# Kernel tuning notes

Hardware: AMD Instinct MI355X
Metric: run time of the kernel (lower is better)

Reference implementation:

```python
import jax, jax.numpy as jnp
import numpy as np


def hard_sigmoid(x):
    # Keras hard_sigmoid: clip(0.2*x + 0.5, 0, 1)
    return jnp.clip(0.2 * x + 0.5, 0.0, 1.0)


def lstm_layer(x, W, U, b):
    """Run a Keras-style LSTM cell over time.

    x: [B, T, D], W: [D, 4H], U: [H, 4H], b: [4H]. Gate order i,f,g,o.
    Returns full hidden sequence [B, T, H].
    """
    B = x.shape[0]
    H = U.shape[0]
    h0 = jnp.zeros((B, H), dtype=x.dtype)
    c0 = jnp.zeros((B, H), dtype=x.dtype)
    # Precompute input projections for all timesteps in one big GEMM.
    xz = jnp.einsum('btd,dk->btk', x, W) + b  # [B, T, 4H]
    xz_t = jnp.swapaxes(xz, 0, 1)             # [T, B, 4H]

    def step(carry, zx_t):
        h, c = carry
        z = zx_t + h @ U                       # [B, 4H]
        i, f, g, o = jnp.split(z, 4, axis=-1)
        i = hard_sigmoid(i)
        f = hard_sigmoid(f)
        g = jnp.tanh(g)
        o = hard_sigmoid(o)
        c = f * c + i * g
        h = o * jnp.tanh(c)
        return (h, c), h

    (_, _), hs = jax.lax.scan(step, (h0, c0), xz_t)  # hs: [T, B, H]
    return jnp.swapaxes(hs, 0, 1)  # [B, T, H]


def setup_inputs() -> dict:
    key = jax.random.key(0)
    ks = jax.random.split(key, 7)
    B, T, D, H = 32, 512, 1024, 1024
    s_in = 1.0 / np.sqrt(D)
    s_h = 1.0 / np.sqrt(H)
    return {
        'x': jax.random.normal(ks[0], (B, T, D), dtype=jnp.float32),
        'W0': jax.random.normal(ks[1], (D, 4 * H), dtype=jnp.float32) * s_in,
        'U0': jax.random.normal(ks[2], (H, 4 * H), dtype=jnp.float32) * s_h,
        'b0': jnp.zeros((4 * H,), dtype=jnp.float32),
        'W1': jax.random.normal(ks[3], (H, 4 * H), dtype=jnp.float32) * s_h,
        'U1': jax.random.normal(ks[4], (H, 4 * H), dtype=jnp.float32) * s_h,
        'b1': jnp.zeros((4 * H,), dtype=jnp.float32),
    }


def reference(x, W0, U0, b0, W1, U1, b1):
    # StackedRNNCells: output of cell 0 at time t feeds cell 1 at time t.
    # Equivalent to running layer 0 over the whole sequence, then layer 1.
    h1 = lstm_layer(x, W0, U0, b0)    # [B, T, H]
    h2 = lstm_layer(h1, W1, U1, b1)   # [B, T, H]
    # RNN(return_sequences=False): last timestep output of the top cell.
    return h2[:, -1, :]
```

## Files before the change

### kernel.cpp

```cpp
#include <hip/hip_runtime.h>
#include <math.h>

#define B_  32
#define T_  512
#define H_  1024
#define G4_ 4096
#define NT  512

typedef __attribute__((ext_vector_type(8))) _Float16 f16x8;
typedef __attribute__((ext_vector_type(4))) float   f32x4;

#define ROWP 1032
#define WROW 264

__device__ __forceinline__ float hardsig(float z) {
    return fminf(fmaxf(0.2f * z + 0.5f, 0.0f), 1.0f);
}
__device__ __forceinline__ float fast_tanh(float x) {
    float ax = fabsf(x);
    float e  = __expf(-2.0f * ax);
    float t  = (1.0f - e) / (1.0f + e);
    return copysignf(t, x);
}
__device__ __forceinline__ unsigned ldA(const unsigned* p) {
    return __hip_atomic_load(p, __ATOMIC_RELAXED, __HIP_MEMORY_SCOPE_AGENT);
}
__device__ __forceinline__ void stA32(unsigned* p, unsigned v) {
    __hip_atomic_store(p, v, __ATOMIC_RELAXED, __HIP_MEMORY_SCOPE_AGENT);
}

__device__ __forceinline__ void load_wfrags(const float* M, int colbase, int myrow,
                                            int koff, bool keep, f16x8* wf, _Float16* st) {
    for (int kc = 0; kc < 4; ++kc) {
        __syncthreads();
        #pragma unroll
        for (int it = 0; it < 4; ++it) {
            int id  = it * NT + (int)threadIdx.x;
            int kl  = id >> 3, gc8 = id & 7;
            int gcol = (gc8 >> 1) * 1024 + colbase + (gc8 & 1) * 8;
            const float* src = M + (size_t)(kc * 256 + kl) * G4_ + gcol;
            float4 v0 = *(const float4*)src;
            float4 v1 = *(const float4*)(src + 4);
            int rb = gc8 * 8;
            st[(rb+0)*WROW+kl]=(_Float16)v0.x; st[(rb+1)*WROW+kl]=(_Float16)v0.y;
            st[(rb+2)*WROW+kl]=(_Float16)v0.z; st[(rb+3)*WROW+kl]=(_Float16)v0.w;
            st[(rb+4)*WROW+kl]=(_Float16)v1.x; st[(rb+5)*WROW+kl]=(_Float16)v1.y;
            st[(rb+6)*WROW+kl]=(_Float16)v1.z; st[(rb+7)*WROW+kl]=(_Float16)v1.w;
        }
        __syncthreads();
        if (keep) {
            #pragma unroll
            for (int kj = 0; kj < 8; ++kj)
                wf[kc*8+kj] = *(const f16x8*)&st[myrow * WROW + kj * 32 + koff];
        }
    }
    __syncthreads();
}

__global__ __launch_bounds__(NT, 1)
void lstm3(const float* __restrict__ x,
           const float* __restrict__ W0, const float* __restrict__ U0, const float* __restrict__ b0,
           const float* __restrict__ W1, const float* __restrict__ U1, const float* __restrict__ b1,
           _Float16* __restrict__ h1,
           _Float16* __restrict__ h2,
           _Float16* __restrict__ xzr,
           const _Float16* __restrict__ zp,
           unsigned* __restrict__ ctr,
           float* __restrict__ out)
{
    __shared__ __align__(16) char smem[149504];
    _Float16* stA  = (_Float16*)smem;
    _Float16* stB  = (_Float16*)(smem + 66048);
    float*    red0 = (float*)(smem + 66048);
    float*    red1 = (float*)(smem + 132096);

    const int tid  = threadIdx.x;
    const int bid  = blockIdx.x;
    const int w    = tid >> 6, l = tid & 63;
    const int koff = (l >> 4) * 8;

    if (bid >= 128) {
        const int e = bid - 128;
        const int gbase = e * 32;
        _Float16* w0l = (_Float16*)smem;

        #pragma unroll 2
        for (int it = 0; it < 8; ++it) {
            int id = it * NT + tid;
            int k = id >> 2, gc8 = id & 3;
            const float* src = W0 + (size_t)k * G4_ + gbase + gc8 * 8;
            float4 v0 = *(const float4*)src;
            float4 v1 = *(const float4*)(src + 4);
            int rb = gc8 * 8;
            w0l[(rb+0)*ROWP+k]=(_Float16)v0.x; w0l[(rb+1)*ROWP+k]=(_Float16)v0.y;
            w0l[(rb+2)*ROWP+k]=(_Float16)v0.z; w0l[(rb+3)*ROWP+k]=(_Float16)v0.w;
            w0l[(rb+4)*ROWP+k]=(_Float16)v1.x; w0l[(rb+5)*ROWP+k]=(_Float16)v1.y;
            w0l[(rb+6)*ROWP+k]=(_Float16)v1.z; w0l[(rb+7)*ROWP+k]=(_Float16)v1.w;
        }
        __syncthreads();

        for (int c = 0; c < 64; ++c) {
            if (c >= 4 && tid == 0) {
                const unsigned need = (unsigned)(8 * c - 24);
                while (ldA(&ctr[64 + (e & 15) * 16]) < need) __builtin_amdgcn_s_sleep(1);
            }
            __syncthreads();

            f32x4 acc[2][2] = {{{0,0,0,0},{0,0,0,0}},{{0,0,0,0},{0,0,0,0}}};
            const float* xrow[2];
            #pragma unroll
            for (int p = 0; p < 2; ++p) {
                const int m  = (w * 2 + p) * 16 + (l & 15);
                const int tl = m >> 5, bb = m & 31;
                xrow[p] = x + ((size_t)bb * T_ + (8 * c + tl)) * 1024;
            }
            #pragma unroll 4
            for (int kiG = 0; kiG < 32; ++kiG) {
                const int kk = kiG * 32 + koff;
                f16x8 bf0 = *(const f16x8*)&w0l[( 0 + (l & 15)) * ROWP + kk];
                f16x8 bf1 = *(const f16x8*)&w0l[(16 + (l & 15)) * ROWP + kk];
                #pragma unroll
                for (int p = 0; p < 2; ++p) {
                    float4 v0 = *(const float4*)&xrow[p][kk];
                    float4 v1 = *(const float4*)&xrow[p][kk + 4];
                    f16x8 af;
                    af[0]=(_Float16)v0.x; af[1]=(_Float16)v0.y; af[2]=(_Float16)v0.z; af[3]=(_Float16)v0.w;
                    af[4]=(_Float16)v1.x; af[5]=(_Float16)v1.y; af[6]=(_Float16)v1.z; af[7]=(_Float16)v1.w;
                    acc[p][0] = __builtin_amdgcn_mfma_f32_16x16x32_f16(af, bf0, acc[p][0], 0, 0, 0);
                    acc[p][1] = __builtin_amdgcn_mfma_f32_16x16x32_f16(af, bf1, acc[p][1], 0, 0, 0);
                }
            }
            #pragma unroll
            for (int p = 0; p < 2; ++p)
                #pragma unroll
                for (int n = 0; n < 2; ++n)
                    #pragma unroll
                    for (int i = 0; i < 4; ++i) {
                        _Float16 hf = (_Float16)acc[p][n][i];
                        unsigned short us; __builtin_memcpy(&us, &hf, 2);
                        unsigned up = us;
                        unsigned op = (unsigned)__shfl_xor((int)up, 1);
                        if (!(l & 1)) {
                            const int m  = (w * 2 + p) * 16 + (l >> 4) * 4 + i;
                            const int tl = m >> 5, bb = m & 31;
                            size_t off = (((size_t)(c & 3) * 8 + tl) * B_ + bb) * G4_
                                       + gbase + n * 16 + (l & 15);
                            stA32((unsigned*)&xzr[off], up | (op << 16));
                        }
                    }
            asm volatile("s_waitcnt vmcnt(0)" ::: "memory");
            __syncthreads();
            if (tid == 0) {
                unsigned old = __hip_atomic_fetch_add(&ctr[32], 1u, __ATOMIC_RELAXED, __HIP_MEMORY_SCOPE_AGENT);
                if ((old & 127u) == 127u) {
                    #pragma unroll
                    for (int i = 0; i < 16; ++i) stA32(&ctr[576 + i * 16], (unsigned)(c + 1));
                }
            }
        }
        return;
    }

    const int dom  = (bid >= 64);
    const int dbid = bid & 63;
    const int jb   = dbid * 16;

    const int bb   = tid >> 4;
    const int jj   = tid & 15;
    const int jcol = jb + jj;

    float bias_[4];
    {
        const float* bl = dom ? b1 : b0;
        #pragma unroll
        for (int g = 0; g < 4; ++g) bias_[g] = bl[(size_t)g * H_ + jcol];
    }
    float creg = 0.f;

    f16x8 wf[32];
    if (dom == 0) {
        const int g = w & 3;
        load_wfrags(U0, jb, g * 16 + (l & 15), koff, true, wf, stA);
    } else {
        const int g = w & 3;
        load_wfrags(W1, jb, g * 16 + (l & 15), koff, (w < 4),  wf, stA);
        load_wfrags(U1, jb, g * 16 + (l & 15), koff, (w >= 4), wf, stA);
    }

    for (int t = 0; t < T_; ++t) {
        if (tid == 0) {
            if (dom == 0) {
                const unsigned xt = (unsigned)((t >> 3) + 1);
                while (ldA(&ctr[576 + (dbid & 15) * 16]) < xt) __builtin_amdgcn_s_sleep(1);
                if (t > 0)
                    while (ldA(&ctr[64 + (dbid & 15) * 16]) < (unsigned)t) __builtin_amdgcn_s_sleep(1);
            } else {
                while (ldA(&ctr[64 + (dbid & 15) * 16]) < (unsigned)(t + 1)) __builtin_amdgcn_s_sleep(1);
                if (t > 0)
                    while (ldA(&ctr[320 + (dbid & 15) * 16]) < (unsigned)t) __builtin_amdgcn_s_sleep(1);
            }
        }
        __syncthreads();

        {
            const int r = tid >> 4, ch = tid & 15;
            if (dom == 0) {
                const _Float16* s1 = (t ? h1 + ((size_t)(t-1) * B_ + r) * H_ : zp + (size_t)r * H_) + ch * 64;
                _Float16* d1 = stA + r * ROWP + ch * 64;
                #pragma unroll
                for (int u = 0; u < 8; ++u) *(uint4*)(d1 + u*8) = *(const uint4*)(s1 + u*8);
            } else {
                const _Float16* s1 = h1 + ((size_t)t * B_ + r) * H_ + ch * 64;
                const _Float16* s2 = (t ? h2 + ((size_t)(t-1) * B_ + r) * H_ : zp + (size_t)r * H_) + ch * 64;
                _Float16* d1 = stA + r * ROWP + ch * 64;
                _Float16* d2 = stB + r * ROWP + ch * 64;
                #pragma unroll
                for (int u = 0; u < 8; ++u) *(uint4*)(d1 + u*8) = *(const uint4*)(s1 + u*8);
                #pragma unroll
                for (int u = 0; u < 8; ++u) *(uint4*)(d2 + u*8) = *(const uint4*)(s2 + u*8);
            }
        }
        float xzv[4] = {0.f, 0.f, 0.f, 0.f};
        if (dom == 0) {
            const size_t base = (((size_t)((t >> 3) & 3) * 8 + (t & 7)) * B_ + bb) * G4_;
            #pragma unroll
            for (int g = 0; g < 4; ++g) {
                const unsigned* dp = (const unsigned*)&xzr[base + g * 1024 + (jcol & ~1)];
                unsigned dv = ldA(dp);
                unsigned short hb = (jcol & 1) ? (unsigned short)(dv >> 16) : (unsigned short)(dv & 0xffff);
                _Float16 hf; __builtin_memcpy(&hf, &hb, 2);
                xzv[g] = (float)hf;
            }
        }
        __syncthreads();

        if (dom == 0) {
            const int mt = w >> 2, g = w & 3;
            const _Float16* ar = stA + (mt * 16 + (l & 15)) * ROWP;
            f32x4 aE = {0,0,0,0}, aO = {0,0,0,0};
            #pragma unroll
            for (int kiG = 0; kiG < 32; kiG += 2) {
                f16x8 a0 = *(const f16x8*)&ar[kiG * 32 + koff];
                f16x8 a1 = *(const f16x8*)&ar[(kiG + 1) * 32 + koff];
                aE = __builtin_amdgcn_mfma_f32_16x16x32_f16(a0, wf[kiG],   aE, 0, 0, 0);
                aO = __builtin_amdgcn_mfma_f32_16x16x32_f16(a1, wf[kiG+1], aO, 0, 0, 0);
            }
            f32x4 acc = aE + aO;
            #pragma unroll
            for (int i = 0; i < 4; ++i)
                red0[((mt * 4 + g) * 16 + (l >> 4) * 4 + i) * 17 + (l & 15)] = acc[i];
        } else {
            const int rl = w >> 2, g = w & 3;
            const _Float16* ab = rl ? stB : stA;
            f32x4 ac0 = {0,0,0,0}, ac1 = {0,0,0,0};
            #pragma unroll
            for (int kiG = 0; kiG < 32; ++kiG) {
                const int kk = kiG * 32 + koff;
                f16x8 bfr = wf[kiG];
                f16x8 a0 = *(const f16x8*)&ab[( 0 + (l & 15)) * ROWP + kk];
                f16x8 a1 = *(const f16x8*)&ab[(16 + (l & 15)) * ROWP + kk];
                ac0 = __builtin_amdgcn_mfma_f32_16x16x32_f16(a0, bfr, ac0, 0, 0, 0);
                ac1 = __builtin_amdgcn_mfma_f32_16x16x32_f16(a1, bfr, ac1, 0, 0, 0);
            }
            #pragma unroll
            for (int i = 0; i < 4; ++i) {
                red1[(((rl * 2 + 0) * 4 + g) * 16 + (l >> 4) * 4 + i) * 17 + (l & 15)] = ac0[i];
                red1[(((rl * 2 + 1) * 4 + g) * 16 + (l >> 4) * 4 + i) * 17 + (l & 15)] = ac1[i];
            }
        }
        __syncthreads();

        {
            float z[4];
            if (dom == 0) {
                #pragma unroll
                for (int g = 0; g < 4; ++g)
                    z[g] = red0[(((bb >> 4) * 4 + g) * 16 + (bb & 15)) * 17 + jj] + xzv[g] + bias_[g];
            } else {
                #pragma unroll
                for (int g = 0; g < 4; ++g)
                    z[g] = red1[(((0 * 2 + (bb >> 4)) * 4 + g) * 16 + (bb & 15)) * 17 + jj]
                         + red1[(((1 * 2 + (bb >> 4)) * 4 + g) * 16 + (bb & 15)) * 17 + jj] + bias_[g];
            }
            float ig = hardsig(z[0]), fg = hardsig(z[1]);
            float gg = fast_tanh(z[2]), og = hardsig(z[3]);
            creg = fg * creg + ig * gg;
            float hval = og * fast_tanh(creg);
            _Float16 hf = (_Float16)hval;
            unsigned short us; __builtin_memcpy(&us, &hf, 2);
            unsigned up = us;
            unsigned op = (unsigned)__shfl_xor((int)up, 1);
            if (!(tid & 1)) {
                unsigned val = up | (op << 16);
                _Float16* arr = dom ? h2 : h1;
                stA32((unsigned*)&arr[((size_t)t * B_ + bb) * H_ + jcol], val);
            }
            if (dom == 1 && t == T_ - 1) out[(size_t)bb * H_ + jcol] = hval;
        }
        asm volatile("s_waitcnt vmcnt(0)" ::: "memory");
        __syncthreads();

        if (tid == 0) {
            unsigned* ap = dom ? &ctr[16] : &ctr[0];
            unsigned old = __hip_atomic_fetch_add(ap, 1u, __ATOMIC_RELAXED, __HIP_MEMORY_SCOPE_AGENT);
            if ((old & 63u) == 63u) {
                unsigned* gp = dom ? &ctr[320] : &ctr[64];
                #pragma unroll
                for (int i = 0; i < 16; ++i) stA32(gp + i * 16, (unsigned)(t + 1));
            }
        }
    }
}

extern "C" void kernel_launch(void* const* d_in, const int* in_sizes, int n_in,
                              void* d_out, int out_size, void* d_ws, size_t ws_size,
                              hipStream_t stream) {
    const float* x  = (const float*)d_in[0];
    const float* W0 = (const float*)d_in[1];
    const float* U0 = (const float*)d_in[2];
    const float* b0 = (const float*)d_in[3];
    const float* W1 = (const float*)d_in[4];
    const float* U1 = (const float*)d_in[5];
    const float* b1 = (const float*)d_in[6];
    float* out = (float*)d_out;

    char* ws = (char*)d_ws;
    const size_t off_h1 = 0;
    const size_t off_h2 = 33554432;
    const size_t off_xz = 67108864;
    const size_t off_zp = 75497472;
    const size_t off_ct = 75563008;

    _Float16* h1  = (_Float16*)(ws + off_h1);
    _Float16* h2  = (_Float16*)(ws + off_h2);
    _Float16* xzr = (_Float16*)(ws + off_xz);
    _Float16* zp  = (_Float16*)(ws + off_zp);
    unsigned* ctr = (unsigned*)(ws + off_ct);

    hipMemsetAsync(ws + off_zp, 0, 65536 + 4096, stream);

    hipLaunchKernelGGL(lstm3, dim3(256), dim3(NT), 0, stream,
                       x, W0, U0, b0, W1, U1, b1,
                       h1, h2, xzr, zp, ctr, out);
}
```

Measured before the change: 3.940 ms.

## Rebalance persistent LSTM blocks and stage weights in LDS fragment layout

The block split changes: 64 blocks run layer 0, 128 blocks run layer 1 with 8 columns each, and 64 blocks compute the input projection with 64 columns each. Weights are now kept in LDS, pre-swizzled into MFMA fragment order, instead of in registers. The per-step copy of h into LDS is removed, and A fragments are read straight from global memory. Barriers become hierarchical two-level atomic counters, and the waiting is split across two lanes using a wave vote. The aim is a shorter critical path per recurrent step; the cost is uncached global reads of h in the inner loop and more counter traffic.

```diff
diff --git a/kernel.cpp b/kernel.cpp
--- a/kernel.cpp
+++ b/kernel.cpp
@@ -10,9 +10,6 @@
 typedef __attribute__((ext_vector_type(8))) _Float16 f16x8;
 typedef __attribute__((ext_vector_type(4))) float   f32x4;
 
-#define ROWP 1032
-#define WROW 264
-
 __device__ __forceinline__ float hardsig(float z) {
     return fminf(fmaxf(0.2f * z + 0.5f, 0.0f), 1.0f);
 }
@@ -29,36 +26,9 @@
     __hip_atomic_store(p, v, __ATOMIC_RELAXED, __HIP_MEMORY_SCOPE_AGENT);
 }
 
-__device__ __forceinline__ void load_wfrags(const float* M, int colbase, int myrow,
-                                            int koff, bool keep, f16x8* wf, _Float16* st) {
-    for (int kc = 0; kc < 4; ++kc) {
-        __syncthreads();
-        #pragma unroll
-        for (int it = 0; it < 4; ++it) {
-            int id  = it * NT + (int)threadIdx.x;
-            int kl  = id >> 3, gc8 = id & 7;
-            int gcol = (gc8 >> 1) * 1024 + colbase + (gc8 & 1) * 8;
-            const float* src = M + (size_t)(kc * 256 + kl) * G4_ + gcol;
-            float4 v0 = *(const float4*)src;
-            float4 v1 = *(const float4*)(src + 4);
-            int rb = gc8 * 8;
-            st[(rb+0)*WROW+kl]=(_Float16)v0.x; st[(rb+1)*WROW+kl]=(_Float16)v0.y;
-            st[(rb+2)*WROW+kl]=(_Float16)v0.z; st[(rb+3)*WROW+kl]=(_Float16)v0.w;
-            st[(rb+4)*WROW+kl]=(_Float16)v1.x; st[(rb+5)*WROW+kl]=(_Float16)v1.y;
-            st[(rb+6)*WROW+kl]=(_Float16)v1.z; st[(rb+7)*WROW+kl]=(_Float16)v1.w;
-        }
-        __syncthreads();
-        if (keep) {
-            #pragma unroll
-            for (int kj = 0; kj < 8; ++kj)
-                wf[kc*8+kj] = *(const f16x8*)&st[myrow * WROW + kj * 32 + koff];
-        }
-    }
-    __syncthreads();
-}
 
 __global__ __launch_bounds__(NT, 1)
-void lstm3(const float* __restrict__ x,
+void lstm8(const float* __restrict__ x,
            const float* __restrict__ W0, const float* __restrict__ U0, const float* __restrict__ b0,
            const float* __restrict__ W1, const float* __restrict__ U1, const float* __restrict__ b1,
            _Float16* __restrict__ h1,
@@ -68,245 +38,288 @@
            unsigned* __restrict__ ctr,
            float* __restrict__ out)
 {
-    __shared__ __align__(16) char smem[149504];
-    _Float16* stA  = (_Float16*)smem;
-    _Float16* stB  = (_Float16*)(smem + 66048);
-    float*    red0 = (float*)(smem + 66048);
-    float*    red1 = (float*)(smem + 132096);
-
-    const int tid  = threadIdx.x;
-    const int bid  = blockIdx.x;
-    const int w    = tid >> 6, l = tid & 63;
+    __shared__ __align__(16) char smem[139776];
+    _Float16* Wl  = (_Float16*)smem;
+    float*    red = (float*)(smem + 131072);
+
+    const int tid = threadIdx.x, bid = blockIdx.x;
+    const int w = tid >> 6, l = tid & 63;
     const int koff = (l >> 4) * 8;
 
-    if (bid >= 128) {
-        const int e = bid - 128;
-        const int gbase = e * 32;
-        _Float16* w0l = (_Float16*)smem;
-
-        #pragma unroll 2
-        for (int it = 0; it < 8; ++it) {
-            int id = it * NT + tid;
-            int k = id >> 2, gc8 = id & 3;
-            const float* src = W0 + (size_t)k * G4_ + gbase + gc8 * 8;
-            float4 v0 = *(const float4*)src;
-            float4 v1 = *(const float4*)(src + 4);
-            int rb = gc8 * 8;
-            w0l[(rb+0)*ROWP+k]=(_Float16)v0.x; w0l[(rb+1)*ROWP+k]=(_Float16)v0.y;
-            w0l[(rb+2)*ROWP+k]=(_Float16)v0.z; w0l[(rb+3)*ROWP+k]=(_Float16)v0.w;
-            w0l[(rb+4)*ROWP+k]=(_Float16)v1.x; w0l[(rb+5)*ROWP+k]=(_Float16)v1.y;
-            w0l[(rb+6)*ROWP+k]=(_Float16)v1.z; w0l[(rb+7)*ROWP+k]=(_Float16)v1.w;
+    if (bid >= 192) {
+        const int e = bid - 192, gbase = e * 64;
+        for (int fi = tid; fi < 16384; fi += NT) {
+            const int k = fi >> 4, rem = fi & 15;
+            const float* src = W0 + (size_t)k * G4_ + gbase + rem * 4;
+            float4 v = *(const float4*)src;
+            const int kiG = k >> 5, jsub = 16 * ((k & 31) >> 3), e8 = k & 7;
+            #pragma unroll
+            for (int c = 0; c < 4; ++c) {
+                const int j = rem * 4 + c, nf = j >> 4, lane = (j & 15) + jsub;
+                float fv = (c == 0) ? v.x : (c == 1) ? v.y : (c == 2) ? v.z : v.w;
+                Wl[((nf * 32 + kiG) * 64 + lane) * 8 + e8] = (_Float16)fv;
+            }
         }
         __syncthreads();
 
         for (int c = 0; c < 64; ++c) {
             if (c >= 4 && tid == 0) {
                 const unsigned need = (unsigned)(8 * c - 24);
-                while (ldA(&ctr[64 + (e & 15) * 16]) < need) __builtin_amdgcn_s_sleep(1);
-            }
-            __syncthreads();
-
-            f32x4 acc[2][2] = {{{0,0,0,0},{0,0,0,0}},{{0,0,0,0},{0,0,0,0}}};
+                while (ldA(&ctr[144 + (e & 15) * 16]) < need) __builtin_amdgcn_s_sleep(1);
+            }
+            __syncthreads();
+
+            f32x4 acc[2][4];
+            #pragma unroll
+            for (int p = 0; p < 2; ++p)
+                #pragma unroll
+                for (int nf = 0; nf < 4; ++nf) acc[p][nf] = (f32x4){0.f, 0.f, 0.f, 0.f};
             const float* xrow[2];
             #pragma unroll
             for (int p = 0; p < 2; ++p) {
-                const int m  = (w * 2 + p) * 16 + (l & 15);
-                const int tl = m >> 5, bb = m & 31;
-                xrow[p] = x + ((size_t)bb * T_ + (8 * c + tl)) * 1024;
+                const int m = (w * 2 + p) * 16 + (l & 15);
+                xrow[p] = x + ((size_t)(m & 31) * T_ + (8 * c + (m >> 5))) * 1024;
             }
             #pragma unroll 4
             for (int kiG = 0; kiG < 32; ++kiG) {
                 const int kk = kiG * 32 + koff;
-                f16x8 bf0 = *(const f16x8*)&w0l[( 0 + (l & 15)) * ROWP + kk];
-                f16x8 bf1 = *(const f16x8*)&w0l[(16 + (l & 15)) * ROWP + kk];
+                f16x8 af[2];
                 #pragma unroll
                 for (int p = 0; p < 2; ++p) {
                     float4 v0 = *(const float4*)&xrow[p][kk];
                     float4 v1 = *(const float4*)&xrow[p][kk + 4];
-                    f16x8 af;
-                    af[0]=(_Float16)v0.x; af[1]=(_Float16)v0.y; af[2]=(_Float16)v0.z; af[3]=(_Float16)v0.w;
-                    af[4]=(_Float16)v1.x; af[5]=(_Float16)v1.y; af[6]=(_Float16)v1.z; af[7]=(_Float16)v1.w;
-                    acc[p][0] = __builtin_amdgcn_mfma_f32_16x16x32_f16(af, bf0, acc[p][0], 0, 0, 0);
-                    acc[p][1] = __builtin_amdgcn_mfma_f32_16x16x32_f16(af, bf1, acc[p][1], 0, 0, 0);
+                    af[p][0]=(_Float16)v0.x; af[p][1]=(_Float16)v0.y;
+                    af[p][2]=(_Float16)v0.z; af[p][3]=(_Float16)v0.w;
+                    af[p][4]=(_Float16)v1.x; af[p][5]=(_Float16)v1.y;
+                    af[p][6]=(_Float16)v1.z; af[p][7]=(_Float16)v1.w;
+                }
+                #pragma unroll
+                for (int nf = 0; nf < 4; ++nf) {
+                    f16x8 bf = *(const f16x8*)&Wl[((nf * 32 + kiG) * 64 + l) * 8];
+                    acc[0][nf] = __builtin_amdgcn_mfma_f32_16x16x32_f16(af[0], bf, acc[0][nf], 0, 0, 0);
+                    acc[1][nf] = __builtin_amdgcn_mfma_f32_16x16x32_f16(af[1], bf, acc[1][nf], 0, 0, 0);
                 }
             }
             #pragma unroll
             for (int p = 0; p < 2; ++p)
                 #pragma unroll
-                for (int n = 0; n < 2; ++n)
+                for (int nf = 0; nf < 4; ++nf)
                     #pragma unroll
                     for (int i = 0; i < 4; ++i) {
-                        _Float16 hf = (_Float16)acc[p][n][i];
+                        _Float16 hf = (_Float16)acc[p][nf][i];
                         unsigned short us; __builtin_memcpy(&us, &hf, 2);
                         unsigned up = us;
                         unsigned op = (unsigned)__shfl_xor((int)up, 1);
                         if (!(l & 1)) {
-                            const int m  = (w * 2 + p) * 16 + (l >> 4) * 4 + i;
-                            const int tl = m >> 5, bb = m & 31;
-                            size_t off = (((size_t)(c & 3) * 8 + tl) * B_ + bb) * G4_
-                                       + gbase + n * 16 + (l & 15);
+                            const int m = (w * 2 + p) * 16 + (l >> 4) * 4 + i;
+                            size_t off = (((size_t)(c & 3) * 8 + (m >> 5)) * B_ + (m & 31)) * G4_
+                                       + gbase + nf * 16 + ((l & 15) & ~1);
                             stA32((unsigned*)&xzr[off], up | (op << 16));
                         }
                     }
             asm volatile("s_waitcnt vmcnt(0)" ::: "memory");
             __syncthreads();
             if (tid == 0) {
-                unsigned old = __hip_atomic_fetch_add(&ctr[32], 1u, __ATOMIC_RELAXED, __HIP_MEMORY_SCOPE_AGENT);
-                if ((old & 127u) == 127u) {
+                unsigned old = __hip_atomic_fetch_add(&ctr[928], 1u, __ATOMIC_RELAXED, __HIP_MEMORY_SCOPE_AGENT);
+                if ((old & 63u) == 63u) {
                     #pragma unroll
-                    for (int i = 0; i < 16; ++i) stA32(&ctr[576 + i * 16], (unsigned)(c + 1));
+                    for (int i = 0; i < 16; ++i) stA32(&ctr[944 + i * 16], (unsigned)(c + 1));
                 }
             }
         }
         return;
     }
 
-    const int dom  = (bid >= 64);
-    const int dbid = bid & 63;
-    const int jb   = dbid * 16;
-
-    const int bb   = tid >> 4;
-    const int jj   = tid & 15;
-    const int jcol = jb + jj;
-
-    float bias_[4];
-    {
-        const float* bl = dom ? b1 : b0;
+    const int dom = (bid >= 64);
+
+    if (dom == 0) {
+        const int jb = bid * 16;
+        for (int fi = tid; fi < 16384; fi += NT) {
+            const int k = fi >> 4, rem = fi & 15, g = rem >> 2, jq = (rem & 3) * 4;
+            const float* src = U0 + (size_t)k * G4_ + g * 1024 + jb + jq;
+            float4 v = *(const float4*)src;
+            const int kiG = k >> 5, jsub = 16 * ((k & 31) >> 3), e8 = k & 7;
+            #pragma unroll
+            for (int c = 0; c < 4; ++c) {
+                const int lane = (jq + c) + jsub;
+                float fv = (c == 0) ? v.x : (c == 1) ? v.y : (c == 2) ? v.z : v.w;
+                Wl[((g * 32 + kiG) * 64 + lane) * 8 + e8] = (_Float16)fv;
+            }
+        }
+        const int bb = tid >> 4, jj = tid & 15, jcol = jb + jj;
+        float bias4[4];
         #pragma unroll
-        for (int g = 0; g < 4; ++g) bias_[g] = bl[(size_t)g * H_ + jcol];
-    }
-    float creg = 0.f;
-
-    f16x8 wf[32];
-    if (dom == 0) {
-        const int g = w & 3;
-        load_wfrags(U0, jb, g * 16 + (l & 15), koff, true, wf, stA);
+        for (int g = 0; g < 4; ++g) bias4[g] = b0[(size_t)g * H_ + jcol];
+        float creg = 0.f;
+        const int mt = w >> 2, g = w & 3;
+        const int arow = mt * 16 + (l & 15);
+        __syncthreads();
+
+        for (int t = 0; t < T_; ++t) {
+            if (tid < 2) {
+                const unsigned* p = tid ? &ctr[144 + (bid & 15) * 16] : &ctr[944 + (bid & 15) * 16];
+                const unsigned tgt = tid ? (unsigned)t : (unsigned)((t >> 3) + 1);
+                bool ok = (tid == 1 && t == 0);
+                while (true) {
+                    ok = ok || (ldA(p) >= tgt);
+                    if (__all((int)ok)) break;
+                    __builtin_amdgcn_s_sleep(1);
+                }
+            }
+            asm volatile("" ::: "memory");
+            __syncthreads();
+
+            unsigned xzd[4];
+            {
+                const size_t xbase = (((size_t)((t >> 3) & 3) * 8 + (t & 7)) * B_ + bb) * G4_;
+                #pragma unroll
+                for (int gg = 0; gg < 4; ++gg)
+                    xzd[gg] = ldA((const unsigned*)&xzr[xbase + gg * 1024 + jb + (jj & ~1)]);
+            }
+
+            const _Float16* hp = t ? h1 + ((size_t)(t - 1) * B_ + arow) * H_
+                                   : zp + (size_t)arow * H_;
+            f32x4 acc = {0.f, 0.f, 0.f, 0.f};
+            #pragma unroll 8
+            for (int kiG = 0; kiG < 32; ++kiG) {
+                f16x8 af = *(const f16x8*)&hp[kiG * 32 + koff];
+                f16x8 bf = *(const f16x8*)&Wl[((g * 32 + kiG) * 64 + l) * 8];
+                acc = __builtin_amdgcn_mfma_f32_16x16x32_f16(af, bf, acc, 0, 0, 0);
+            }
+            #pragma unroll
+            for (int i = 0; i < 4; ++i)
+                red[((mt * 4 + g) * 16 + (l >> 4) * 4 + i) * 17 + (l & 15)] = acc[i];
+            __syncthreads();
+
+            {
+                float z[4];
+                #pragma unroll
+                for (int gg = 0; gg < 4; ++gg) {
+                    float xv;
+                    {
+                        unsigned dv = xzd[gg];
+                        unsigned short hb = (jj & 1) ? (unsigned short)(dv >> 16) : (unsigned short)(dv & 0xffffu);
+                        _Float16 hf; __builtin_memcpy(&hf, &hb, 2);
+                        xv = (float)hf;
+                    }
+                    z[gg] = red[(((bb >> 4) * 4 + gg) * 16 + (bb & 15)) * 17 + jj] + xv + bias4[gg];
+                }
+                float ig = hardsig(z[0]), fg = hardsig(z[1]);
+                float gg2 = fast_tanh(z[2]), og = hardsig(z[3]);
+                creg = fg * creg + ig * gg2;
+                float hval = og * fast_tanh(creg);
+                _Float16 hf = (_Float16)hval;
+                unsigned short us; __builtin_memcpy(&us, &hf, 2);
+                unsigned up = us;
+                unsigned op = (unsigned)__shfl_xor((int)up, 1);
+                if (!(tid & 1))
+                    stA32((unsigned*)&h1[((size_t)t * B_ + bb) * H_ + (jcol & ~1)], up | (op << 16));
+            }
+            asm volatile("s_waitcnt vmcnt(0)" ::: "memory");
+            __syncthreads();
+
+            if (tid == 0) {
+                unsigned old = __hip_atomic_fetch_add(&ctr[(bid >> 3) * 16], 1u, __ATOMIC_RELAXED, __HIP_MEMORY_SCOPE_AGENT);
+                if ((old & 7u) == 7u) {
+                    unsigned r = __hip_atomic_fetch_add(&ctr[128], 1u, __ATOMIC_RELAXED, __HIP_MEMORY_SCOPE_AGENT);
+                    if ((r & 7u) == 7u) {
+                        #pragma unroll
+                        for (int i = 0; i < 16; ++i) stA32(&ctr[144 + i * 16], (unsigned)(t + 1));
+                    }
+                }
+            }
+        }
     } else {
-        const int g = w & 3;
-        load_wfrags(W1, jb, g * 16 + (l & 15), koff, (w < 4),  wf, stA);
-        load_wfrags(U1, jb, g * 16 + (l & 15), koff, (w >= 4), wf, stA);
-    }
-
-    for (int t = 0; t < T_; ++t) {
-        if (tid == 0) {
-            if (dom == 0) {
-                const unsigned xt = (unsigned)((t >> 3) + 1);
-                while (ldA(&ctr[576 + (dbid & 15) * 16]) < xt) __builtin_amdgcn_s_sleep(1);
-                if (t > 0)
-                    while (ldA(&ctr[64 + (dbid & 15) * 16]) < (unsigned)t) __builtin_amdgcn_s_sleep(1);
-            } else {
-                while (ldA(&ctr[64 + (dbid & 15) * 16]) < (unsigned)(t + 1)) __builtin_amdgcn_s_sleep(1);
-                if (t > 0)
-                    while (ldA(&ctr[320 + (dbid & 15) * 16]) < (unsigned)t) __builtin_amdgcn_s_sleep(1);
-            }
-        }
+        const int db = bid - 64, jb8 = db * 8;
+        for (int m = 0; m < 2; ++m) {
+            const float* M = m ? U1 : W1;
+            for (int fi = tid; fi < 8192; fi += NT) {
+                const int k = fi >> 3, rem = fi & 7, g = rem >> 1, jq = (rem & 1) * 4;
+                const float* src = M + (size_t)k * G4_ + g * 1024 + jb8 + jq;
+                float4 v = *(const float4*)src;
+                const int kiG = k >> 5, jsub = 16 * ((k & 31) >> 3), e8 = k & 7;
+                #pragma unroll
+                for (int c = 0; c < 4; ++c) {
+                    const int j = g * 8 + jq + c, nf = j >> 4, lane = (j & 15) + jsub;
+                    float fv = (c == 0) ? v.x : (c == 1) ? v.y : (c == 2) ? v.z : v.w;
+                    Wl[(((m * 2 + nf) * 32 + kiG) * 64 + lane) * 8 + e8] = (_Float16)fv;
+                }
+            }
+        }
+        const int bb = tid >> 3, jj = tid & 7, jcol = jb8 + jj;
+        float bias4[4];
+        if (tid < 256) {
+            #pragma unroll
+            for (int g = 0; g < 4; ++g) bias4[g] = b1[(size_t)g * H_ + jcol];
+        }
+        float creg = 0.f;
+        const int role = w >> 2, mt = (w >> 1) & 1, nf = w & 1;
+        const int arow = mt * 16 + (l & 15);
         __syncthreads();
 
-        {
-            const int r = tid >> 4, ch = tid & 15;
-            if (dom == 0) {
-                const _Float16* s1 = (t ? h1 + ((size_t)(t-1) * B_ + r) * H_ : zp + (size_t)r * H_) + ch * 64;
-                _Float16* d1 = stA + r * ROWP + ch * 64;
-                #pragma unroll
-                for (int u = 0; u < 8; ++u) *(uint4*)(d1 + u*8) = *(const uint4*)(s1 + u*8);
-            } else {
-                const _Float16* s1 = h1 + ((size_t)t * B_ + r) * H_ + ch * 64;
-                const _Float16* s2 = (t ? h2 + ((size_t)(t-1) * B_ + r) * H_ : zp + (size_t)r * H_) + ch * 64;
-                _Float16* d1 = stA + r * ROWP + ch * 64;
-                _Float16* d2 = stB + r * ROWP + ch * 64;
-                #pragma unroll
-                for (int u = 0; u < 8; ++u) *(uint4*)(d1 + u*8) = *(const uint4*)(s1 + u*8);
-                #pragma unroll
-                for (int u = 0; u < 8; ++u) *(uint4*)(d2 + u*8) = *(const uint4*)(s2 + u*8);
-            }
-        }
-        float xzv[4] = {0.f, 0.f, 0.f, 0.f};
-        if (dom == 0) {
-            const size_t base = (((size_t)((t >> 3) & 3) * 8 + (t & 7)) * B_ + bb) * G4_;
-            #pragma unroll
-            for (int g = 0; g < 4; ++g) {
-                const unsigned* dp = (const unsigned*)&xzr[base + g * 1024 + (jcol & ~1)];
-                unsigned dv = ldA(dp);
-                unsigned short hb = (jcol & 1) ? (unsigned short)(dv >> 16) : (unsigned short)(dv & 0xffff);
-                _Float16 hf; __builtin_memcpy(&hf, &hb, 2);
-                xzv[g] = (float)hf;
-            }
-        }
-        __syncthreads();
-
-        if (dom == 0) {
-            const int mt = w >> 2, g = w & 3;
-            const _Float16* ar = stA + (mt * 16 + (l & 15)) * ROWP;
-            f32x4 aE = {0,0,0,0}, aO = {0,0,0,0};
-            #pragma unroll
-            for (int kiG = 0; kiG < 32; kiG += 2) {
-                f16x8 a0 = *(const f16x8*)&ar[kiG * 32 + koff];
-                f16x8 a1 = *(const f16x8*)&ar[(kiG + 1) * 32 + koff];
-                aE = __builtin_amdgcn_mfma_f32_16x16x32_f16(a0, wf[kiG],   aE, 0, 0, 0);
-                aO = __builtin_amdgcn_mfma_f32_16x16x32_f16(a1, wf[kiG+1], aO, 0, 0, 0);
-            }
-            f32x4 acc = aE + aO;
+        for (int t = 0; t < T_; ++t) {
+            if (tid < 2) {
+                const unsigned* p = tid ? &ctr[672 + (db & 15) * 16] : &ctr[144 + (db & 15) * 16];
+                const unsigned tgt = tid ? (unsigned)t : (unsigned)(t + 1);
+                bool ok = (tid == 1 && t == 0);
+                while (true) {
+                    ok = ok || (ldA(p) >= tgt);
+                    if (__all((int)ok)) break;
+                    __builtin_amdgcn_s_sleep(1);
+                }
+            }
+            asm volatile("" ::: "memory");
+            __syncthreads();
+
+            const _Float16* hp;
+            if (role == 0) hp = h1 + ((size_t)t * B_ + arow) * H_;
+            else           hp = t ? h2 + ((size_t)(t - 1) * B_ + arow) * H_
+                                  : zp + (size_t)arow * H_;
+            f32x4 acc = {0.f, 0.f, 0.f, 0.f};
+            #pragma unroll 8
+            for (int kiG = 0; kiG < 32; ++kiG) {
+                f16x8 af = *(const f16x8*)&hp[kiG * 32 + koff];
+                f16x8 bf = *(const f16x8*)&Wl[(((role * 2 + nf) * 32 + kiG) * 64 + l) * 8];
+                acc = __builtin_amdgcn_mfma_f32_16x16x32_f16(af, bf, acc, 0, 0, 0);
+            }
             #pragma unroll
             for (int i = 0; i < 4; ++i)
-                red0[((mt * 4 + g) * 16 + (l >> 4) * 4 + i) * 17 + (l & 15)] = acc[i];
-        } else {
-            const int rl = w >> 2, g = w & 3;
-            const _Float16* ab = rl ? stB : stA;
-            f32x4 ac0 = {0,0,0,0}, ac1 = {0,0,0,0};
-            #pragma unroll
-            for (int kiG = 0; kiG < 32; ++kiG) {
-                const int kk = kiG * 32 + koff;
-                f16x8 bfr = wf[kiG];
-                f16x8 a0 = *(const f16x8*)&ab[( 0 + (l & 15)) * ROWP + kk];
-                f16x8 a1 = *(const f16x8*)&ab[(16 + (l & 15)) * ROWP + kk];
-                ac0 = __builtin_amdgcn_mfma_f32_16x16x32_f16(a0, bfr, ac0, 0, 0, 0);
-                ac1 = __builtin_amdgcn_mfma_f32_16x16x32_f16(a1, bfr, ac1, 0, 0, 0);
-            }
-            #pragma unroll
-            for (int i = 0; i < 4; ++i) {
-                red1[(((rl * 2 + 0) * 4 + g) * 16 + (l >> 4) * 4 + i) * 17 + (l & 15)] = ac0[i];
-                red1[(((rl * 2 + 1) * 4 + g) * 16 + (l >> 4) * 4 + i) * 17 + (l & 15)] = ac1[i];
-            }
-        }
-        __syncthreads();
-
-        {
-            float z[4];
-            if (dom == 0) {
-                #pragma unroll
-                for (int g = 0; g < 4; ++g)
-                    z[g] = red0[(((bb >> 4) * 4 + g) * 16 + (bb & 15)) * 17 + jj] + xzv[g] + bias_[g];
-            } else {
-                #pragma unroll
-                for (int g = 0; g < 4; ++g)
-                    z[g] = red1[(((0 * 2 + (bb >> 4)) * 4 + g) * 16 + (bb & 15)) * 17 + jj]
-                         + red1[(((1 * 2 + (bb >> 4)) * 4 + g) * 16 + (bb & 15)) * 17 + jj] + bias_[g];
-            }
-            float ig = hardsig(z[0]), fg = hardsig(z[1]);
-            float gg = fast_tanh(z[2]), og = hardsig(z[3]);
-            creg = fg * creg + ig * gg;
-            float hval = og * fast_tanh(creg);
-            _Float16 hf = (_Float16)hval;
-            unsigned short us; __builtin_memcpy(&us, &hf, 2);
-            unsigned up = us;
-            unsigned op = (unsigned)__shfl_xor((int)up, 1);
-            if (!(tid & 1)) {
-                unsigned val = up | (op << 16);
-                _Float16* arr = dom ? h2 : h1;
-                stA32((unsigned*)&arr[((size_t)t * B_ + bb) * H_ + jcol], val);
-            }
-            if (dom == 1 && t == T_ - 1) out[(size_t)bb * H_ + jcol] = hval;
-        }
-        asm volatile("s_waitcnt vmcnt(0)" ::: "memory");
-        __syncthreads();
-
-        if (tid == 0) {
-            unsigned* ap = dom ? &ctr[16] : &ctr[0];
-            unsigned old = __hip_atomic_fetch_add(ap, 1u, __ATOMIC_RELAXED, __HIP_MEMORY_SCOPE_AGENT);
-            if ((old & 63u) == 63u) {
-                unsigned* gp = dom ? &ctr[320] : &ctr[64];
-                #pragma unroll
-                for (int i = 0; i < 16; ++i) stA32(gp + i * 16, (unsigned)(t + 1));
+                red[((role * 4 + mt * 2 + nf) * 16 + (l >> 4) * 4 + i) * 17 + (l & 15)] = acc[i];
+            __syncthreads();
+
+            if (tid < 256) {
+                const int rmt = bb >> 4, row = bb & 15;
+                float z[4];
+                #pragma unroll
+                for (int g = 0; g < 4; ++g) {
+                    const int j = g * 8 + jj, nff = j >> 4, col = j & 15;
+                    z[g] = red[((0 * 4 + rmt * 2 + nff) * 16 + row) * 17 + col]
+                         + red[((1 * 4 + rmt * 2 + nff) * 16 + row) * 17 + col] + bias4[g];
+                }
+                float ig = hardsig(z[0]), fg = hardsig(z[1]);
+                float gg2 = fast_tanh(z[2]), og = hardsig(z[3]);
+                creg = fg * creg + ig * gg2;
+                float hval = og * fast_tanh(creg);
+                _Float16 hf = (_Float16)hval;
+                unsigned short us; __builtin_memcpy(&us, &hf, 2);
+                unsigned up = us;
+                unsigned op = (unsigned)__shfl_xor((int)up, 1);
+                if (!(tid & 1))
+                    stA32((unsigned*)&h2[((size_t)t * B_ + bb) * H_ + (jcol & ~1)], up | (op << 16));
+                if (t == T_ - 1) out[(size_t)bb * H_ + jcol] = hval;
+            }
+            asm volatile("s_waitcnt vmcnt(0)" ::: "memory");
+            __syncthreads();
+
+            if (tid == 0) {
+                unsigned old = __hip_atomic_fetch_add(&ctr[400 + (db >> 3) * 16], 1u, __ATOMIC_RELAXED, __HIP_MEMORY_SCOPE_AGENT);
+                if ((old & 7u) == 7u) {
+                    unsigned r = __hip_atomic_fetch_add(&ctr[656], 1u, __ATOMIC_RELAXED, __HIP_MEMORY_SCOPE_AGENT);
+                    if ((r & 15u) == 15u) {
+                        #pragma unroll
+                        for (int i = 0; i < 16; ++i) stA32(&ctr[672 + i * 16], (unsigned)(t + 1));
+                    }
+                }
             }
         }
     }
@@ -337,9 +350,9 @@
     _Float16* zp  = (_Float16*)(ws + off_zp);
     unsigned* ctr = (unsigned*)(ws + off_ct);
 
-    hipMemsetAsync(ws + off_zp, 0, 65536 + 4096, stream);
-
-    hipLaunchKernelGGL(lstm3, dim3(256), dim3(NT), 0, stream,
+    hipMemsetAsync(ws + off_zp, 0, 65536 + 8192, stream);
+
+    hipLaunchKernelGGL(lstm8, dim3(256), dim3(NT), 0, stream,
                        x, W0, U0, b0, W1, U1, b1,
                        h1, h2, xzr, zp, ctr, out);
 }
```

Measured after the change: 5.098 ms. 1.29x slower.
